# Kernel optimization log

Hardware: AMD Instinct MI355X
Metric: run time of the kernel (lower is better)

## Reference

```python
import jax, jax.numpy as jnp
import numpy as np

GROUP_SIZE = 128
INTERMEDIATE = 18944


def _unpack_int4(packed):
    # packed: [rows, cols//8] int32, 8 nibbles per int32 along output dim
    shifts = jnp.arange(8, dtype=jnp.int32) * 4
    nib = (packed[:, :, None] >> shifts) & 15  # [rows, cols//8, 8]
    return nib.reshape(packed.shape[0], packed.shape[1] * 8)


def awq_gemm(x, qweight, qzeros, scales, group_size):
    # Dequantize: W[i,j] = (w4[i,j] - z4[i//g, j]) * scales[i//g, j]
    w = _unpack_int4(qweight).astype(jnp.float32)           # [in, out]
    z = _unpack_int4(qzeros).astype(jnp.float32)            # [in//g, out]
    s = scales.astype(jnp.float32)                          # [in//g, out]
    W = ((w - jnp.repeat(z, group_size, axis=0)) * jnp.repeat(s, group_size, axis=0))
    return (x @ W.astype(x.dtype))                          # [tokens, out]


def setup_inputs() -> dict:
    key = jax.random.key(0)
    ks = jax.random.split(key, 7)
    imax = 2147483647
    return {
        "x": (jax.random.normal(ks[0], (4096, 3584), dtype=jnp.float32) * 0.02).astype(jnp.float16),
        "qweight_gu": jax.random.randint(ks[1], (3584, 4736), 0, imax, dtype=jnp.int32),
        "qzeros_gu": jax.random.randint(ks[2], (28, 4736), 0, imax, dtype=jnp.int32),
        "scales_gu": (jax.random.uniform(ks[3], (28, 37888), dtype=jnp.float32) * 0.01 + 0.001).astype(jnp.float16),
        "qweight_down": jax.random.randint(ks[4], (18944, 448), 0, imax, dtype=jnp.int32),
        "qzeros_down": jax.random.randint(ks[5], (148, 448), 0, imax, dtype=jnp.int32),
        "scales_down": (jax.random.uniform(ks[6], (148, 3584), dtype=jnp.float32) * 0.01 + 0.001).astype(jnp.float16),
    }


def reference(x, qweight_gu, qzeros_gu, scales_gu, qweight_down, qzeros_down, scales_down):
    # Fused gate+up AWQ GEMM (matches forward path after fuse_gate_up())
    gate_up = awq_gemm(x, qweight_gu, qzeros_gu, scales_gu, GROUP_SIZE)  # [T, 2*I]
    gate = gate_up[..., :INTERMEDIATE]
    up = gate_up[..., INTERMEDIATE:]
    intermediate = jax.nn.silu(gate) * up                                # fused SiLU*mul
    down = awq_gemm(intermediate, qweight_down, qzeros_down, scales_down, GROUP_SIZE)
    return down
```

## Files before the change

### kernel.cpp

```cpp
#include <hip/hip_runtime.h>
#include <hip/hip_fp16.h>
#include <stdint.h>

typedef _Float16 half8 __attribute__((ext_vector_type(8)));
typedef _Float16 h2v __attribute__((ext_vector_type(2)));
typedef float f32x4 __attribute__((ext_vector_type(4)));

#define GLD_LDS16(gp, lp)                                                     \
  __builtin_amdgcn_global_load_lds(                                           \
      (const __attribute__((address_space(1))) void*)(gp),                    \
      (__attribute__((address_space(3))) void*)(lp), 16, 0, 0)
#define GLD_LDS4(gp, lp)                                                      \
  __builtin_amdgcn_global_load_lds(                                           \
      (const __attribute__((address_space(1))) void*)(gp),                    \
      (__attribute__((address_space(3))) void*)(lp), 4, 0, 0)

__global__ void xcvt_kernel(const float* __restrict__ in, __half* __restrict__ out) {
  const size_t i = ((size_t)blockIdx.x * 256 + threadIdx.x) * 4;
  float4 v = *(const float4*)(in + i);
  __half2* o = (__half2*)(out + i);
  o[0] = __floats2half2_rn(v.x, v.y);
  o[1] = __floats2half2_rn(v.z, v.w);
}

__global__ void repack_kernel(const int* __restrict__ qw, uint32_t* __restrict__ rp, int P) {
  const int N = P * 8;
  const int n = blockIdx.x * 256 + threadIdx.x;
  const int j8 = n >> 3;
  const int sh = (n & 7) * 4;
  #pragma unroll
  for (int qi = 0; qi < 4; ++qi) {
    const int q = blockIdx.y * 4 + qi;
    const int* src = qw + (size_t)(q * 8) * P + j8;
    uint32_t r = 0;
    #pragma unroll
    for (int t = 0; t < 8; ++t) {
      uint32_t w = ((uint32_t)src[t * P] >> sh) & 15u;
      r |= w << (4 * (t >> 1) + 16 * (t & 1));
    }
    rp[(size_t)q * N + n] = r;
  }
}

__global__ void smz_kernel(const float* __restrict__ sc, const int* __restrict__ qz,
                           uint32_t* __restrict__ smz, int P) {
  const int N = P * 8;
  const int n = blockIdx.x * 256 + threadIdx.x;
  const int g = blockIdx.y;
  uint32_t sbits = __half_as_ushort(__float2half(sc[(size_t)g * N + n]));
  uint32_t z = ((uint32_t)qz[(size_t)g * P + (n >> 3)] >> ((n & 7) * 4)) & 15u;
  uint32_t hz = 0x6400u | z;
  smz[(size_t)g * N + n] = sbits | (hz << 16);
}

union U32H2 { uint32_t u; h2v h; };
__device__ inline h2v bith2(uint32_t u) { U32H2 t; t.u = u; return t.h; }
__device__ inline uint32_t h2bit(h2v h) { U32H2 t; t.h = h; return t.u; }
__device__ inline half8 dequant8(uint32_t p, h2v s, h2v z) {
  union { uint32_t u[4]; half8 v; } r;
  r.u[0] = h2bit((bith2((p & 0x000F000Fu) | 0x64006400u) - z) * s);
  r.u[1] = h2bit((bith2(((p >> 4) & 0x000F000Fu) | 0x64006400u) - z) * s);
  r.u[2] = h2bit((bith2(((p >> 8) & 0x000F000Fu) | 0x64006400u) - z) * s);
  r.u[3] = h2bit((bith2(((p >> 12) & 0x000F000Fu) | 0x64006400u) - z) * s);
  return r.v;
}

template <int KDIM, int NW, int T1OFF, int OW, bool SILU, int NT, int BXS>
__global__ __launch_bounds__(256, 2) void awq_gemm(const __half* __restrict__ A,
                                                   const uint32_t* __restrict__ RP,
                                                   const uint32_t* __restrict__ SMZ,
                                                   void* __restrict__ OUT) {
  constexpr int ABUF = 128 * 64 * 2;
  constexpr int BBUF = NT * 8 * 128 * 4;
  constexpr int BOFF = 3 * ABUF;
  constexpr int ZOFF = BOFF + 3 * BBUF;
  __shared__ __align__(16) unsigned char smem[ZOFF + 2048];

  const int tid = threadIdx.x;
  const int l = tid & 63;
  const int wv = tid >> 6;
  const int l15 = l & 15;
  const int l4 = l >> 4;

  const int row0 = blockIdx.y * 128;
  const int n0 = blockIdx.x * BXS;

  const __half* asrc[4];
  #pragma unroll
  for (int it = 0; it < 4; ++it) {
    int m = it * 32 + (tid >> 3);
    int cs = tid & 7;
    int kc = cs ^ (m & 7);
    asrc[it] = A + (size_t)(row0 + m) * KDIM + kc * 8;
  }

  const uint32_t* bsrc[NT];
  #pragma unroll
  for (int it = 0; it < NT; ++it) {
    int idx = it * 256 + tid;
    int tile = idx >> 8;
    int qr = (idx >> 5) & 7;
    int l32 = idx & 31;
    int S = ((qr & 1) << 4) | ((qr >> 1) << 2);
    bsrc[it] = RP + (size_t)qr * NW + n0 + tile * T1OFF + ((l32 * 4) ^ S);
  }

  const uint32_t* zsrc = SMZ + n0 + (size_t)(tid >> 7) * T1OFF + (tid & 127);

  f32x4 acc[NT][2][8];
  const f32x4 zero4 = {0.f, 0.f, 0.f, 0.f};
  #pragma unroll
  for (int t = 0; t < NT; ++t)
    #pragma unroll
    for (int nf = 0; nf < 2; ++nf)
      #pragma unroll
      for (int mf = 0; mf < 8; ++mf) acc[t][nf][mf] = zero4;

  uint32_t s2[NT][2], z2[NT][2];
  constexpr int NSTEP = KDIM / 64;

  #pragma unroll
  for (int it = 0; it < 4; ++it)
    GLD_LDS16(asrc[it], &smem[it * 4096 + tid * 16]);
  #pragma unroll
  for (int it = 0; it < NT; ++it)
    GLD_LDS16(bsrc[it], &smem[BOFF + (it * 256 + tid) * 16]);
  GLD_LDS4(zsrc, &smem[ZOFF + tid * 4]);
  #pragma unroll
  for (int it = 0; it < 4; ++it)
    GLD_LDS16(asrc[it] + 64, &smem[ABUF + it * 4096 + tid * 16]);
  #pragma unroll
  for (int it = 0; it < NT; ++it)
    GLD_LDS16(bsrc[it] + (size_t)8 * NW, &smem[BOFF + BBUF + (it * 256 + tid) * 16]);

  int cur = 0, stg = 2;
  for (int t = 0; t < NSTEP; ++t) {
    if (t == NSTEP - 1)      asm volatile("s_waitcnt vmcnt(0)" ::: "memory");
    else if (t & 1)          asm volatile("s_waitcnt vmcnt(7)" ::: "memory");
    else                     asm volatile("s_waitcnt vmcnt(6)" ::: "memory");
    __builtin_amdgcn_s_barrier();

    if (t + 2 < NSTEP) {
      #pragma unroll
      for (int it = 0; it < 4; ++it)
        GLD_LDS16(asrc[it] + (size_t)(t + 2) * 64, &smem[stg * ABUF + it * 4096 + tid * 16]);
      #pragma unroll
      for (int it = 0; it < NT; ++it)
        GLD_LDS16(bsrc[it] + (size_t)(t + 2) * 8 * NW,
                  &smem[BOFF + stg * BBUF + (it * 256 + tid) * 16]);
      if (((t + 2) & 1) == 0) {
        const int g = (t + 2) >> 1;
        GLD_LDS4(zsrc + (size_t)g * NW, &smem[ZOFF + (g & 1) * 1024 + tid * 4]);
      }
    }

    if ((t & 1) == 0) {
      const uint32_t* zl = (const uint32_t*)&smem[ZOFF + ((t >> 1) & 1) * 1024];
      #pragma unroll
      for (int tile = 0; tile < NT; ++tile)
        #pragma unroll
        for (int nf = 0; nf < 2; ++nf) {
          uint32_t u = zl[tile * 128 + wv * 32 + nf * 16 + l15];
          uint32_t lo = u & 0xFFFFu;
          s2[tile][nf] = lo | (lo << 16);
          z2[tile][nf] = (u & 0xFFFF0000u) | (u >> 16);
        }
    }

    uint32_t bq[2][NT][2];
    const int bro = wv * 32 + l15;
    const unsigned char* bbase = &smem[BOFF + cur * BBUF];
    #pragma unroll
    for (int kk = 0; kk < 2; ++kk) {
      const int Sl = ((l4 & 1) << 4) | (kk << 3) | ((l4 >> 1) << 2);
      #pragma unroll
      for (int tile = 0; tile < NT; ++tile)
        #pragma unroll
        for (int nf = 0; nf < 2; ++nf)
          bq[kk][tile][nf] = *(const uint32_t*)&bbase[
              (((tile * 8 + kk * 4 + l4) * 128) + ((bro + nf * 16) ^ Sl)) * 4];
    }

    const unsigned char* abase = &smem[cur * ABUF];
    __builtin_amdgcn_s_setprio(1);
    #pragma unroll
    for (int kk = 0; kk < 2; ++kk) {
      half8 a[8];
      #pragma unroll
      for (int mf = 0; mf < 8; ++mf) {
        int m = mf * 16 + l15;
        int chunk = (kk * 4 + l4) ^ (l15 & 7);
        a[mf] = *(const half8*)(abase + m * 128 + chunk * 16);
      }
      #pragma unroll
      for (int tile = 0; tile < NT; ++tile)
        #pragma unroll
        for (int nf = 0; nf < 2; ++nf) {
          half8 b = dequant8(bq[kk][tile][nf], bith2(s2[tile][nf]), bith2(z2[tile][nf]));
          #pragma unroll
          for (int mf = 0; mf < 8; ++mf)
            acc[tile][nf][mf] =
                __builtin_amdgcn_mfma_f32_16x16x32_f16(a[mf], b, acc[tile][nf][mf], 0, 0, 0);
        }
    }
    __builtin_amdgcn_s_setprio(0);

    cur = (cur == 2) ? 0 : cur + 1;
    stg = (stg == 2) ? 0 : stg + 1;
  }

  if (SILU) {
    __half* O = (__half*)OUT;
    #pragma unroll
    for (int nf = 0; nf < 2; ++nf)
      #pragma unroll
      for (int mf = 0; mf < 8; ++mf)
        #pragma unroll
        for (int r = 0; r < 4; ++r) {
          int row = row0 + mf * 16 + l4 * 4 + r;
          int col = n0 + wv * 32 + nf * 16 + l15;
          float gf = __half2float(__float2half(acc[0][nf][mf][r]));
          float uf = __half2float(__float2half(acc[1][nf][mf][r]));
          float sig = 1.f / (1.f + __expf(-gf));
          float sil = __half2float(__float2half(gf * sig));
          O[(size_t)row * OW + col] = __float2half(sil * uf);
        }
  } else {
    float* O = (float*)OUT;
    #pragma unroll
    for (int tile = 0; tile < NT; ++tile)
      #pragma unroll
      for (int nf = 0; nf < 2; ++nf)
        #pragma unroll
        for (int mf = 0; mf < 8; ++mf)
          #pragma unroll
          for (int r = 0; r < 4; ++r) {
            int row = row0 + mf * 16 + l4 * 4 + r;
            int col = n0 + tile * T1OFF + wv * 32 + nf * 16 + l15;
            O[(size_t)row * OW + col] = __half2float(__float2half(acc[tile][nf][mf][r]));
          }
  }
}

extern "C" void kernel_launch(void* const* d_in, const int* in_sizes, int n_in,
                              void* d_out, int out_size, void* d_ws, size_t ws_size,
                              hipStream_t stream) {
  const float* x_f32 = (const float*)d_in[0];
  const int* qw_gu = (const int*)d_in[1];
  const int* qz_gu = (const int*)d_in[2];
  const float* sc_gu = (const float*)d_in[3];
  const int* qw_dn = (const int*)d_in[4];
  const int* qz_dn = (const int*)d_in[5];
  const float* sc_dn = (const float*)d_in[6];

  char* ws = (char*)d_ws;
  __half* interm   = (__half*)ws;
  uint32_t* rp_gu  = (uint32_t*)(ws + 155189248ull);
  uint32_t* smz_gu = (uint32_t*)(ws + 223084544ull);
  __half* xh       = (__half*)(ws + 227328000ull);
  uint32_t* rp_dn  = (uint32_t*)(ws + 155189248ull);
  uint32_t* smz_dn = (uint32_t*)(ws + 189136896ull);

  xcvt_kernel<<<14336, 256, 0, stream>>>(x_f32, xh);
  repack_kernel<<<dim3(148, 112), 256, 0, stream>>>(qw_gu, rp_gu, 4736);
  smz_kernel<<<dim3(148, 28), 256, 0, stream>>>(sc_gu, qz_gu, smz_gu, 4736);

  awq_gemm<3584, 37888, 18944, 18944, true, 2, 128>
      <<<dim3(148, 32), 256, 0, stream>>>(xh, rp_gu, smz_gu, (void*)interm);

  repack_kernel<<<dim3(14, 592), 256, 0, stream>>>(qw_dn, rp_dn, 448);
  smz_kernel<<<dim3(14, 148), 256, 0, stream>>>(sc_dn, qz_dn, smz_dn, 448);

  awq_gemm<18944, 3584, 128, 3584, false, 2, 256>
      <<<dim3(14, 32), 256, 0, stream>>>(interm, rp_dn, smz_dn, d_out);
}
```

Baseline: 1.609 ms.

## Switch AWQ GEMM inner loop to 32x32x16 MFMA with simplified B layout

```diff
diff --git a/kernel.cpp b/kernel.cpp
--- a/kernel.cpp
+++ b/kernel.cpp
@@ -4,7 +4,7 @@
 
 typedef _Float16 half8 __attribute__((ext_vector_type(8)));
 typedef _Float16 h2v __attribute__((ext_vector_type(2)));
-typedef float f32x4 __attribute__((ext_vector_type(4)));
+typedef float f32x16 __attribute__((ext_vector_type(16)));
 
 #define GLD_LDS16(gp, lp)                                                     \
   __builtin_amdgcn_global_load_lds(                                           \
@@ -79,8 +79,8 @@
   const int tid = threadIdx.x;
   const int l = tid & 63;
   const int wv = tid >> 6;
-  const int l15 = l & 15;
-  const int l4 = l >> 4;
+  const int l31 = l & 31;
+  const int lh = l >> 5;
 
   const int row0 = blockIdx.y * 128;
   const int n0 = blockIdx.x * BXS;
@@ -96,42 +96,39 @@
 
   const uint32_t* bsrc[NT];
   #pragma unroll
-  for (int it = 0; it < NT; ++it) {
-    int idx = it * 256 + tid;
-    int tile = idx >> 8;
-    int qr = (idx >> 5) & 7;
-    int l32 = idx & 31;
-    int S = ((qr & 1) << 4) | ((qr >> 1) << 2);
-    bsrc[it] = RP + (size_t)qr * NW + n0 + tile * T1OFF + ((l32 * 4) ^ S);
-  }
+  for (int tl = 0; tl < NT; ++tl)
+    bsrc[tl] = RP + (size_t)((tid >> 5) & 7) * NW + n0 + tl * T1OFF + (tid & 31) * 4;
 
   const uint32_t* zsrc = SMZ + n0 + (size_t)(tid >> 7) * T1OFF + (tid & 127);
 
-  f32x4 acc[NT][2][8];
-  const f32x4 zero4 = {0.f, 0.f, 0.f, 0.f};
-  #pragma unroll
-  for (int t = 0; t < NT; ++t)
-    #pragma unroll
-    for (int nf = 0; nf < 2; ++nf)
-      #pragma unroll
-      for (int mf = 0; mf < 8; ++mf) acc[t][nf][mf] = zero4;
-
-  uint32_t s2[NT][2], z2[NT][2];
+  f32x16 acc[NT][4];
+  #pragma unroll
+  for (int tl = 0; tl < NT; ++tl)
+    #pragma unroll
+    for (int rf = 0; rf < 4; ++rf)
+      #pragma unroll
+      for (int e = 0; e < 16; ++e) acc[tl][rf][e] = 0.f;
+
+  uint32_t s2[NT], z2[NT];
   constexpr int NSTEP = KDIM / 64;
+
+  const int bbase_l = (wv * 32 + l31) * 4;
+  const int achunk_x = l31 & 7;
+  const int arow_off = l31 * 128;
 
   #pragma unroll
   for (int it = 0; it < 4; ++it)
     GLD_LDS16(asrc[it], &smem[it * 4096 + tid * 16]);
   #pragma unroll
-  for (int it = 0; it < NT; ++it)
-    GLD_LDS16(bsrc[it], &smem[BOFF + (it * 256 + tid) * 16]);
+  for (int tl = 0; tl < NT; ++tl)
+    GLD_LDS16(bsrc[tl], &smem[BOFF + tl * 4096 + tid * 16]);
   GLD_LDS4(zsrc, &smem[ZOFF + tid * 4]);
   #pragma unroll
   for (int it = 0; it < 4; ++it)
     GLD_LDS16(asrc[it] + 64, &smem[ABUF + it * 4096 + tid * 16]);
   #pragma unroll
-  for (int it = 0; it < NT; ++it)
-    GLD_LDS16(bsrc[it] + (size_t)8 * NW, &smem[BOFF + BBUF + (it * 256 + tid) * 16]);
+  for (int tl = 0; tl < NT; ++tl)
+    GLD_LDS16(bsrc[tl] + (size_t)8 * NW, &smem[BOFF + BBUF + tl * 4096 + tid * 16]);
 
   int cur = 0, stg = 2;
   for (int t = 0; t < NSTEP; ++t) {
@@ -145,9 +142,9 @@
       for (int it = 0; it < 4; ++it)
         GLD_LDS16(asrc[it] + (size_t)(t + 2) * 64, &smem[stg * ABUF + it * 4096 + tid * 16]);
       #pragma unroll
-      for (int it = 0; it < NT; ++it)
-        GLD_LDS16(bsrc[it] + (size_t)(t + 2) * 8 * NW,
-                  &smem[BOFF + stg * BBUF + (it * 256 + tid) * 16]);
+      for (int tl = 0; tl < NT; ++tl)
+        GLD_LDS16(bsrc[tl] + (size_t)(t + 2) * 8 * NW,
+                  &smem[BOFF + stg * BBUF + tl * 4096 + tid * 16]);
       if (((t + 2) & 1) == 0) {
         const int g = (t + 2) >> 1;
         GLD_LDS4(zsrc + (size_t)g * NW, &smem[ZOFF + (g & 1) * 1024 + tid * 4]);
@@ -157,53 +154,39 @@
     if ((t & 1) == 0) {
       const uint32_t* zl = (const uint32_t*)&smem[ZOFF + ((t >> 1) & 1) * 1024];
       #pragma unroll
-      for (int tile = 0; tile < NT; ++tile)
+      for (int tl = 0; tl < NT; ++tl) {
+        uint32_t u = zl[tl * 128 + wv * 32 + l31];
+        uint32_t lo = u & 0xFFFFu;
+        s2[tl] = lo | (lo << 16);
+        z2[tl] = (u & 0xFFFF0000u) | (u >> 16);
+      }
+    }
+
+    uint32_t bq[NT][4];
+    const unsigned char* bbase = &smem[BOFF + cur * BBUF];
+    #pragma unroll
+    for (int tl = 0; tl < NT; ++tl)
+      #pragma unroll
+      for (int kf = 0; kf < 4; ++kf)
+        bq[tl][kf] = *(const uint32_t*)&bbase[tl * 4096 + (kf * 2 + lh) * 512 + bbase_l];
+
+    const unsigned char* abase = &smem[cur * ABUF];
+    #pragma unroll
+    for (int kf = 0; kf < 4; ++kf) {
+      half8 a[4];
+      const int chunk = ((kf * 2 + lh) ^ achunk_x) * 16;
+      #pragma unroll
+      for (int rf = 0; rf < 4; ++rf)
+        a[rf] = *(const half8*)(abase + rf * 4096 + arow_off + chunk);
+      #pragma unroll
+      for (int tl = 0; tl < NT; ++tl) {
+        half8 b = dequant8(bq[tl][kf], bith2(s2[tl]), bith2(z2[tl]));
         #pragma unroll
-        for (int nf = 0; nf < 2; ++nf) {
-          uint32_t u = zl[tile * 128 + wv * 32 + nf * 16 + l15];
-          uint32_t lo = u & 0xFFFFu;
-          s2[tile][nf] = lo | (lo << 16);
-          z2[tile][nf] = (u & 0xFFFF0000u) | (u >> 16);
-        }
-    }
-
-    uint32_t bq[2][NT][2];
-    const int bro = wv * 32 + l15;
-    const unsigned char* bbase = &smem[BOFF + cur * BBUF];
-    #pragma unroll
-    for (int kk = 0; kk < 2; ++kk) {
-      const int Sl = ((l4 & 1) << 4) | (kk << 3) | ((l4 >> 1) << 2);
-      #pragma unroll
-      for (int tile = 0; tile < NT; ++tile)
-        #pragma unroll
-        for (int nf = 0; nf < 2; ++nf)
-          bq[kk][tile][nf] = *(const uint32_t*)&bbase[
-              (((tile * 8 + kk * 4 + l4) * 128) + ((bro + nf * 16) ^ Sl)) * 4];
-    }
-
-    const unsigned char* abase = &smem[cur * ABUF];
-    __builtin_amdgcn_s_setprio(1);
-    #pragma unroll
-    for (int kk = 0; kk < 2; ++kk) {
-      half8 a[8];
-      #pragma unroll
-      for (int mf = 0; mf < 8; ++mf) {
-        int m = mf * 16 + l15;
-        int chunk = (kk * 4 + l4) ^ (l15 & 7);
-        a[mf] = *(const half8*)(abase + m * 128 + chunk * 16);
-      }
-      #pragma unroll
-      for (int tile = 0; tile < NT; ++tile)
-        #pragma unroll
-        for (int nf = 0; nf < 2; ++nf) {
-          half8 b = dequant8(bq[kk][tile][nf], bith2(s2[tile][nf]), bith2(z2[tile][nf]));
-          #pragma unroll
-          for (int mf = 0; mf < 8; ++mf)
-            acc[tile][nf][mf] =
-                __builtin_amdgcn_mfma_f32_16x16x32_f16(a[mf], b, acc[tile][nf][mf], 0, 0, 0);
-        }
-    }
-    __builtin_amdgcn_s_setprio(0);
+        for (int rf = 0; rf < 4; ++rf)
+          acc[tl][rf] =
+              __builtin_amdgcn_mfma_f32_32x32x16_f16(a[rf], b, acc[tl][rf], 0, 0, 0);
+      }
+    }
 
     cur = (cur == 2) ? 0 : cur + 1;
     stg = (stg == 2) ? 0 : stg + 1;
@@ -212,33 +195,29 @@
   if (SILU) {
     __half* O = (__half*)OUT;
     #pragma unroll
-    for (int nf = 0; nf < 2; ++nf)
-      #pragma unroll
-      for (int mf = 0; mf < 8; ++mf)
-        #pragma unroll
-        for (int r = 0; r < 4; ++r) {
-          int row = row0 + mf * 16 + l4 * 4 + r;
-          int col = n0 + wv * 32 + nf * 16 + l15;
-          float gf = __half2float(__float2half(acc[0][nf][mf][r]));
-          float uf = __half2float(__float2half(acc[1][nf][mf][r]));
-          float sig = 1.f / (1.f + __expf(-gf));
-          float sil = __half2float(__float2half(gf * sig));
-          O[(size_t)row * OW + col] = __float2half(sil * uf);
-        }
+    for (int rf = 0; rf < 4; ++rf)
+      #pragma unroll
+      for (int reg = 0; reg < 16; ++reg) {
+        int row = row0 + rf * 32 + (reg & 3) + 8 * (reg >> 2) + 4 * lh;
+        int col = n0 + wv * 32 + l31;
+        float gf = __half2float(__float2half(acc[0][rf][reg]));
+        float uf = __half2float(__float2half(acc[1][rf][reg]));
+        float sig = 1.f / (1.f + __expf(-gf));
+        float sil = __half2float(__float2half(gf * sig));
+        O[(size_t)row * OW + col] = __float2half(sil * uf);
+      }
   } else {
     float* O = (float*)OUT;
     #pragma unroll
-    for (int tile = 0; tile < NT; ++tile)
-      #pragma unroll
-      for (int nf = 0; nf < 2; ++nf)
+    for (int tl = 0; tl < NT; ++tl)
+      #pragma unroll
+      for (int rf = 0; rf < 4; ++rf)
         #pragma unroll
-        for (int mf = 0; mf < 8; ++mf)
-          #pragma unroll
-          for (int r = 0; r < 4; ++r) {
-            int row = row0 + mf * 16 + l4 * 4 + r;
-            int col = n0 + tile * T1OFF + wv * 32 + nf * 16 + l15;
-            O[(size_t)row * OW + col] = __half2float(__float2half(acc[tile][nf][mf][r]));
-          }
+        for (int reg = 0; reg < 16; ++reg) {
+          int row = row0 + rf * 32 + (reg & 3) + 8 * (reg >> 2) + 4 * lh;
+          int col = n0 + tl * T1OFF + wv * 32 + l31;
+          O[(size_t)row * OW + col] = __half2float(__float2half(acc[tl][rf][reg]));
+        }
   }
 }
 
```

New measurement: 1.715 ms. 1.07x slower.

## Split GEMM block tile across 8 waves with fewer accumulators per wave

Applied to the files above, without the earlier changes.

```diff
diff --git a/kernel.cpp b/kernel.cpp
--- a/kernel.cpp
+++ b/kernel.cpp
@@ -65,13 +65,13 @@
   return r.v;
 }
 
-template <int KDIM, int NW, int T1OFF, int OW, bool SILU, int NT, int BXS>
-__global__ __launch_bounds__(256, 2) void awq_gemm(const __half* __restrict__ A,
+template <int KDIM, int NW, int T1OFF, int OW, bool SILU, int BXS>
+__global__ __launch_bounds__(512, 4) void awq_gemm(const __half* __restrict__ A,
                                                    const uint32_t* __restrict__ RP,
                                                    const uint32_t* __restrict__ SMZ,
                                                    void* __restrict__ OUT) {
   constexpr int ABUF = 128 * 64 * 2;
-  constexpr int BBUF = NT * 8 * 128 * 4;
+  constexpr int BBUF = 8 * 256 * 4;
   constexpr int BOFF = 3 * ABUF;
   constexpr int ZOFF = BOFF + 3 * BBUF;
   __shared__ __align__(16) unsigned char smem[ZOFF + 2048];
@@ -81,127 +81,109 @@
   const int wv = tid >> 6;
   const int l15 = l & 15;
   const int l4 = l >> 4;
+  const int wc = wv * 16;
 
   const int row0 = blockIdx.y * 128;
   const int n0 = blockIdx.x * BXS;
 
-  const __half* asrc[4];
-  #pragma unroll
-  for (int it = 0; it < 4; ++it) {
-    int m = it * 32 + (tid >> 3);
+  const __half* asrc[2];
+  #pragma unroll
+  for (int it = 0; it < 2; ++it) {
+    int m = it * 64 + (tid >> 3);
     int cs = tid & 7;
     int kc = cs ^ (m & 7);
     asrc[it] = A + (size_t)(row0 + m) * KDIM + kc * 8;
   }
 
-  const uint32_t* bsrc[NT];
-  #pragma unroll
-  for (int it = 0; it < NT; ++it) {
-    int idx = it * 256 + tid;
-    int tile = idx >> 8;
-    int qr = (idx >> 5) & 7;
-    int l32 = idx & 31;
+  const uint32_t* bsrc;
+  {
+    int qr = tid >> 6;
+    int c4 = (tid & 63) * 4;
     int S = ((qr & 1) << 4) | ((qr >> 1) << 2);
-    bsrc[it] = RP + (size_t)qr * NW + n0 + tile * T1OFF + ((l32 * 4) ^ S);
-  }
-
-  const uint32_t* zsrc = SMZ + n0 + (size_t)(tid >> 7) * T1OFF + (tid & 127);
-
-  f32x4 acc[NT][2][8];
+    int cS = c4 ^ S;
+    int bcol = (cS < 128) ? n0 + cS : n0 + T1OFF + (cS - 128);
+    bsrc = RP + (size_t)qr * NW + bcol;
+  }
+
+  const uint32_t* zsrc;
+  {
+    int w3 = wv & 3;
+    int zc = w3 * 64 + l;
+    zsrc = SMZ + ((zc < 128) ? n0 + zc : n0 + T1OFF + (zc - 128));
+  }
+  const int zdst = ZOFF + (wv & 3) * 256;
+
+  f32x4 acc0[8], acc1[8];
   const f32x4 zero4 = {0.f, 0.f, 0.f, 0.f};
   #pragma unroll
-  for (int t = 0; t < NT; ++t)
-    #pragma unroll
-    for (int nf = 0; nf < 2; ++nf)
-      #pragma unroll
-      for (int mf = 0; mf < 8; ++mf) acc[t][nf][mf] = zero4;
-
-  uint32_t s2[NT][2], z2[NT][2];
+  for (int mf = 0; mf < 8; ++mf) { acc0[mf] = zero4; acc1[mf] = zero4; }
+
+  uint32_t s2[2], z2[2];
   constexpr int NSTEP = KDIM / 64;
 
   #pragma unroll
-  for (int it = 0; it < 4; ++it)
-    GLD_LDS16(asrc[it], &smem[it * 4096 + tid * 16]);
-  #pragma unroll
-  for (int it = 0; it < NT; ++it)
-    GLD_LDS16(bsrc[it], &smem[BOFF + (it * 256 + tid) * 16]);
-  GLD_LDS4(zsrc, &smem[ZOFF + tid * 4]);
-  #pragma unroll
-  for (int it = 0; it < 4; ++it)
-    GLD_LDS16(asrc[it] + 64, &smem[ABUF + it * 4096 + tid * 16]);
-  #pragma unroll
-  for (int it = 0; it < NT; ++it)
-    GLD_LDS16(bsrc[it] + (size_t)8 * NW, &smem[BOFF + BBUF + (it * 256 + tid) * 16]);
+  for (int it = 0; it < 2; ++it)
+    GLD_LDS16(asrc[it], &smem[it * 8192 + tid * 16]);
+  GLD_LDS16(bsrc, &smem[BOFF + tid * 16]);
+  GLD_LDS4(zsrc, &smem[zdst]);
+  #pragma unroll
+  for (int it = 0; it < 2; ++it)
+    GLD_LDS16(asrc[it] + 64, &smem[ABUF + it * 8192 + tid * 16]);
+  GLD_LDS16(bsrc + (size_t)8 * NW, &smem[BOFF + BBUF + tid * 16]);
 
   int cur = 0, stg = 2;
   for (int t = 0; t < NSTEP; ++t) {
     if (t == NSTEP - 1)      asm volatile("s_waitcnt vmcnt(0)" ::: "memory");
-    else if (t & 1)          asm volatile("s_waitcnt vmcnt(7)" ::: "memory");
-    else                     asm volatile("s_waitcnt vmcnt(6)" ::: "memory");
+    else if (t & 1)          asm volatile("s_waitcnt vmcnt(4)" ::: "memory");
+    else                     asm volatile("s_waitcnt vmcnt(3)" ::: "memory");
     __builtin_amdgcn_s_barrier();
 
     if (t + 2 < NSTEP) {
       #pragma unroll
-      for (int it = 0; it < 4; ++it)
-        GLD_LDS16(asrc[it] + (size_t)(t + 2) * 64, &smem[stg * ABUF + it * 4096 + tid * 16]);
-      #pragma unroll
-      for (int it = 0; it < NT; ++it)
-        GLD_LDS16(bsrc[it] + (size_t)(t + 2) * 8 * NW,
-                  &smem[BOFF + stg * BBUF + (it * 256 + tid) * 16]);
+      for (int it = 0; it < 2; ++it)
+        GLD_LDS16(asrc[it] + (size_t)(t + 2) * 64,
+                  &smem[stg * ABUF + it * 8192 + tid * 16]);
+      GLD_LDS16(bsrc + (size_t)(t + 2) * 8 * NW, &smem[BOFF + stg * BBUF + tid * 16]);
       if (((t + 2) & 1) == 0) {
         const int g = (t + 2) >> 1;
-        GLD_LDS4(zsrc + (size_t)g * NW, &smem[ZOFF + (g & 1) * 1024 + tid * 4]);
+        GLD_LDS4(zsrc + (size_t)g * NW, &smem[zdst + (g & 1) * 1024]);
       }
     }
 
     if ((t & 1) == 0) {
       const uint32_t* zl = (const uint32_t*)&smem[ZOFF + ((t >> 1) & 1) * 1024];
-      #pragma unroll
-      for (int tile = 0; tile < NT; ++tile)
-        #pragma unroll
-        for (int nf = 0; nf < 2; ++nf) {
-          uint32_t u = zl[tile * 128 + wv * 32 + nf * 16 + l15];
-          uint32_t lo = u & 0xFFFFu;
-          s2[tile][nf] = lo | (lo << 16);
-          z2[tile][nf] = (u & 0xFFFF0000u) | (u >> 16);
-        }
-    }
-
-    uint32_t bq[2][NT][2];
-    const int bro = wv * 32 + l15;
-    const unsigned char* bbase = &smem[BOFF + cur * BBUF];
+      uint32_t u0 = zl[wc + l15];
+      uint32_t u1 = zl[128 + wc + l15];
+      uint32_t lo0 = u0 & 0xFFFFu, lo1 = u1 & 0xFFFFu;
+      s2[0] = lo0 | (lo0 << 16);
+      z2[0] = (u0 & 0xFFFF0000u) | (u0 >> 16);
+      s2[1] = lo1 | (lo1 << 16);
+      z2[1] = (u1 & 0xFFFF0000u) | (u1 >> 16);
+    }
+
+    uint32_t bq[2][2];
+    const uint32_t* bdw = (const uint32_t*)&smem[BOFF + cur * BBUF];
     #pragma unroll
     for (int kk = 0; kk < 2; ++kk) {
       const int Sl = ((l4 & 1) << 4) | (kk << 3) | ((l4 >> 1) << 2);
-      #pragma unroll
-      for (int tile = 0; tile < NT; ++tile)
-        #pragma unroll
-        for (int nf = 0; nf < 2; ++nf)
-          bq[kk][tile][nf] = *(const uint32_t*)&bbase[
-              (((tile * 8 + kk * 4 + l4) * 128) + ((bro + nf * 16) ^ Sl)) * 4];
+      const int qrow = (kk * 4 + l4) * 256;
+      bq[kk][0] = bdw[qrow + ((wc + l15) ^ Sl)];
+      bq[kk][1] = bdw[qrow + ((128 + wc + l15) ^ Sl)];
     }
 
     const unsigned char* abase = &smem[cur * ABUF];
     __builtin_amdgcn_s_setprio(1);
     #pragma unroll
     for (int kk = 0; kk < 2; ++kk) {
-      half8 a[8];
+      half8 b0 = dequant8(bq[kk][0], bith2(s2[0]), bith2(z2[0]));
+      half8 b1 = dequant8(bq[kk][1], bith2(s2[1]), bith2(z2[1]));
+      const int chunkoff = ((kk * 4 + l4) ^ (l15 & 7)) * 16;
       #pragma unroll
       for (int mf = 0; mf < 8; ++mf) {
-        int m = mf * 16 + l15;
-        int chunk = (kk * 4 + l4) ^ (l15 & 7);
-        a[mf] = *(const half8*)(abase + m * 128 + chunk * 16);
-      }
-      #pragma unroll
-      for (int tile = 0; tile < NT; ++tile)
-        #pragma unroll
-        for (int nf = 0; nf < 2; ++nf) {
-          half8 b = dequant8(bq[kk][tile][nf], bith2(s2[tile][nf]), bith2(z2[tile][nf]));
-          #pragma unroll
-          for (int mf = 0; mf < 8; ++mf)
-            acc[tile][nf][mf] =
-                __builtin_amdgcn_mfma_f32_16x16x32_f16(a[mf], b, acc[tile][nf][mf], 0, 0, 0);
-        }
+        half8 a = *(const half8*)(abase + (mf * 16 + l15) * 128 + chunkoff);
+        acc0[mf] = __builtin_amdgcn_mfma_f32_16x16x32_f16(a, b0, acc0[mf], 0, 0, 0);
+        acc1[mf] = __builtin_amdgcn_mfma_f32_16x16x32_f16(a, b1, acc1[mf], 0, 0, 0);
+      }
     }
     __builtin_amdgcn_s_setprio(0);
 
@@ -212,33 +194,29 @@
   if (SILU) {
     __half* O = (__half*)OUT;
     #pragma unroll
-    for (int nf = 0; nf < 2; ++nf)
-      #pragma unroll
-      for (int mf = 0; mf < 8; ++mf)
-        #pragma unroll
-        for (int r = 0; r < 4; ++r) {
-          int row = row0 + mf * 16 + l4 * 4 + r;
-          int col = n0 + wv * 32 + nf * 16 + l15;
-          float gf = __half2float(__float2half(acc[0][nf][mf][r]));
-          float uf = __half2float(__float2half(acc[1][nf][mf][r]));
-          float sig = 1.f / (1.f + __expf(-gf));
-          float sil = __half2float(__float2half(gf * sig));
-          O[(size_t)row * OW + col] = __float2half(sil * uf);
-        }
+    for (int mf = 0; mf < 8; ++mf)
+      #pragma unroll
+      for (int r = 0; r < 4; ++r) {
+        int row = row0 + mf * 16 + l4 * 4 + r;
+        int col = n0 + wc + l15;
+        float gf = __half2float(__float2half(acc0[mf][r]));
+        float uf = __half2float(__float2half(acc1[mf][r]));
+        float sig = 1.f / (1.f + __expf(-gf));
+        float sil = __half2float(__float2half(gf * sig));
+        O[(size_t)row * OW + col] = __float2half(sil * uf);
+      }
   } else {
     float* O = (float*)OUT;
     #pragma unroll
-    for (int tile = 0; tile < NT; ++tile)
-      #pragma unroll
-      for (int nf = 0; nf < 2; ++nf)
-        #pragma unroll
-        for (int mf = 0; mf < 8; ++mf)
-          #pragma unroll
-          for (int r = 0; r < 4; ++r) {
-            int row = row0 + mf * 16 + l4 * 4 + r;
-            int col = n0 + tile * T1OFF + wv * 32 + nf * 16 + l15;
-            O[(size_t)row * OW + col] = __half2float(__float2half(acc[tile][nf][mf][r]));
-          }
+    for (int mf = 0; mf < 8; ++mf)
+      #pragma unroll
+      for (int r = 0; r < 4; ++r) {
+        int row = row0 + mf * 16 + l4 * 4 + r;
+        int col0 = n0 + wc + l15;
+        int col1 = n0 + T1OFF + wc + l15;
+        O[(size_t)row * OW + col0] = __half2float(__float2half(acc0[mf][r]));
+        O[(size_t)row * OW + col1] = __half2float(__float2half(acc1[mf][r]));
+      }
   }
 }
 
@@ -265,12 +243,12 @@
   repack_kernel<<<dim3(148, 112), 256, 0, stream>>>(qw_gu, rp_gu, 4736);
   smz_kernel<<<dim3(148, 28), 256, 0, stream>>>(sc_gu, qz_gu, smz_gu, 4736);
 
-  awq_gemm<3584, 37888, 18944, 18944, true, 2, 128>
-      <<<dim3(148, 32), 256, 0, stream>>>(xh, rp_gu, smz_gu, (void*)interm);
+  awq_gemm<3584, 37888, 18944, 18944, true, 128>
+      <<<dim3(148, 32), 512, 0, stream>>>(xh, rp_gu, smz_gu, (void*)interm);
 
   repack_kernel<<<dim3(14, 592), 256, 0, stream>>>(qw_dn, rp_dn, 448);
   smz_kernel<<<dim3(14, 148), 256, 0, stream>>>(sc_dn, qz_dn, smz_dn, 448);
 
-  awq_gemm<18944, 3584, 128, 3584, false, 2, 256>
-      <<<dim3(14, 32), 256, 0, stream>>>(interm, rp_dn, smz_dn, d_out);
-}
+  awq_gemm<18944, 3584, 128, 3584, false, 256>
+      <<<dim3(14, 32), 512, 0, stream>>>(interm, rp_dn, smz_dn, d_out);
+}
```

New measurement: 1.630 ms. No clear change (+1.3%).
